# Performance work log

Measured on AMD Instinct MI355X. Metric: run time of the kernel, lower is better.

The kernel has to match this reference:

```python
import jax, jax.numpy as jnp
import numpy as np
import math

N_EMBD = 1024
N_HEAD = 16
B, T = 2, 2048


def new_gelu(x):
    # GPT-2 tanh-approx GELU (matches torch module exactly)
    return 0.5 * x * (1.0 + jnp.tanh(jnp.sqrt(2.0 / jnp.pi) * (x + 0.044715 * x ** 3)))


def layer_norm(x, w, b, eps=1e-5):
    mu = jnp.mean(x, axis=-1, keepdims=True)
    var = jnp.var(x, axis=-1, keepdims=True)
    return (x - mu) * jax.lax.rsqrt(var + eps) * w + b


def setup_inputs() -> dict:
    key = jax.random.key(0)
    ks = jax.random.split(key, 8)
    C = N_EMBD
    s = 0.02
    return {
        "x": jax.random.normal(ks[0], (B, T, C), dtype=jnp.float32),
        "ln1_w": jnp.ones((C,), jnp.float32),
        "ln1_b": jnp.zeros((C,), jnp.float32),
        "attn_w": s * jax.random.normal(ks[1], (C, 3 * C), jnp.float32),
        "attn_b": jnp.zeros((3 * C,), jnp.float32),
        "attn_proj_w": s * jax.random.normal(ks[2], (C, C), jnp.float32),
        "attn_proj_b": jnp.zeros((C,), jnp.float32),
        "ln2_w": jnp.ones((C,), jnp.float32),
        "ln2_b": jnp.zeros((C,), jnp.float32),
        "fc_w": s * jax.random.normal(ks[3], (C, 4 * C), jnp.float32),
        "fc_b": jnp.zeros((4 * C,), jnp.float32),
        "mlp_proj_w": s * jax.random.normal(ks[4], (4 * C, C), jnp.float32),
        "mlp_proj_b": jnp.zeros((C,), jnp.float32),
    }


def block_forward(x, ln1_w, ln1_b, attn_w, attn_b, attn_proj_w, attn_proj_b,
                  ln2_w, ln2_b, fc_w, fc_b, mlp_proj_w, mlp_proj_b):
    Bm, Tm, C = x.shape
    H = N_HEAD
    D = C // H
    # --- self attention (pre-LN) ---
    h = layer_norm(x, ln1_w, ln1_b)
    qkv = h @ attn_w + attn_b  # [B,T,3C]
    q, k, v = jnp.split(qkv, 3, axis=-1)
    q = q.reshape(Bm, Tm, H, D).transpose(0, 2, 1, 3)  # [B,H,T,D]
    k = k.reshape(Bm, Tm, H, D).transpose(0, 2, 1, 3)
    v = v.reshape(Bm, Tm, H, D).transpose(0, 2, 1, 3)
    att = jnp.einsum('bhqd,bhkd->bhqk', q, k) * (1.0 / math.sqrt(D))
    att = jax.nn.softmax(att, axis=-1)  # NOTE: no causal mask in source
    y = jnp.einsum('bhqk,bhkd->bhqd', att, v)
    y = y.transpose(0, 2, 1, 3).reshape(Bm, Tm, C)
    x = x + (y @ attn_proj_w + attn_proj_b)
    # --- MLP ---
    h = layer_norm(x, ln2_w, ln2_b)
    h = new_gelu(h @ fc_w + fc_b)
    x = x + (h @ mlp_proj_w + mlp_proj_b)
    return x


def reference(x, ln1_w, ln1_b, attn_w, attn_b, attn_proj_w, attn_proj_b,
              ln2_w, ln2_b, fc_w, fc_b, mlp_proj_w, mlp_proj_b):
    return block_forward(x, ln1_w, ln1_b, attn_w, attn_b, attn_proj_w, attn_proj_b,
                         ln2_w, ln2_b, fc_w, fc_b, mlp_proj_w, mlp_proj_b)
```

## Files before the change

### kernel.cpp

```cpp
#include <hip/hip_runtime.h>

typedef __attribute__((ext_vector_type(4)))  float  f32x4;
typedef __attribute__((ext_vector_type(16))) float  f32x16;
typedef __attribute__((ext_vector_type(8)))  short  s16x8;
typedef __attribute__((ext_vector_type(4)))  short  s16x4;
typedef __attribute__((ext_vector_type(4)))  unsigned u32x4;
typedef __attribute__((ext_vector_type(2)))  unsigned u32x2;
typedef __attribute__((ext_vector_type(2)))  int    i32x2;

__device__ __forceinline__ short f2bf(float f) {
    unsigned u = __builtin_bit_cast(unsigned, f);
    u += 0x7fff + ((u >> 16) & 1);
    return (short)(u >> 16);
}

__device__ __forceinline__ void load_lds16(const void* g, void* l) {
    __builtin_amdgcn_global_load_lds(
        (const __attribute__((address_space(1))) unsigned int*)g,
        (__attribute__((address_space(3))) unsigned int*)l, 16, 0, 0);
}

__device__ __forceinline__ float tmax32(const f32x16& a, const f32x16& b) {
    float u[11];
#pragma unroll
    for (int i = 0; i < 5; i++)
        u[i] = fmaxf(fmaxf(a[3 * i], a[3 * i + 1]), a[3 * i + 2]);
    u[5] = fmaxf(a[15], b[0]);
#pragma unroll
    for (int i = 0; i < 5; i++)
        u[6 + i] = fmaxf(fmaxf(b[3 * i + 1], b[3 * i + 2]), b[3 * i + 3]);
    float v0 = fmaxf(fmaxf(u[0], u[1]), u[2]);
    float v1 = fmaxf(fmaxf(u[3], u[4]), u[5]);
    float v2 = fmaxf(fmaxf(u[6], u[7]), u[8]);
    float v3 = fmaxf(u[9], u[10]);
    return fmaxf(fmaxf(v0, v1), fmaxf(v2, v3));
}

__device__ __forceinline__ float tsum32(const f32x16& a, const f32x16& b) {
    float u[16];
#pragma unroll
    for (int i = 0; i < 16; i++) u[i] = a[i] + b[i];
#pragma unroll
    for (int i = 0; i < 8; i++) u[i] += u[i + 8];
#pragma unroll
    for (int i = 0; i < 4; i++) u[i] += u[i + 4];
    return (u[0] + u[2]) + (u[1] + u[3]);
}

__global__ __launch_bounds__(256) void transpose_cast(const float* __restrict__ W,
                                                      short* __restrict__ Wt,
                                                      int K, int N) {
    __shared__ float t[32][33];
    int n0 = blockIdx.x * 32, k0 = blockIdx.y * 32;
    int tx = threadIdx.x & 31, ty = threadIdx.x >> 5;
#pragma unroll
    for (int i = 0; i < 4; i++)
        t[ty + 8 * i][tx] = W[(size_t)(k0 + ty + 8 * i) * N + n0 + tx];
    __syncthreads();
#pragma unroll
    for (int i = 0; i < 4; i++)
        Wt[(size_t)(n0 + ty + 8 * i) * K + k0 + tx] = f2bf(t[tx][ty + 8 * i]);
}

__global__ __launch_bounds__(256) void vtrans_kernel(const short* __restrict__ qkv,
                                                     short* __restrict__ Vtg) {
    const int T = 2048, C3 = 3072;
    __shared__ short tl[32][33];
    int bh = blockIdx.y >> 1;
    int b = bh >> 4, h = bh & 15;
    int dh = (blockIdx.y & 1) * 32;
    int t0 = blockIdx.x * 32;
    int tx = threadIdx.x & 31, ty = threadIdx.x >> 5;
    const short* src = qkv + (size_t)b * T * C3 + 2048 + h * 64 + dh;
#pragma unroll
    for (int i = 0; i < 4; i++)
        tl[ty + 8 * i][tx] = src[(size_t)(t0 + ty + 8 * i) * C3 + tx];
    __syncthreads();
#pragma unroll
    for (int i = 0; i < 4; i++)
        Vtg[((size_t)bh * 64 + dh + ty + 8 * i) * T + t0 + tx] = tl[tx][ty + 8 * i];
}

__global__ __launch_bounds__(256) void ln_kernel(const float* __restrict__ x,
                                                 const float* __restrict__ w,
                                                 const float* __restrict__ b,
                                                 short* __restrict__ out) {
    int row = blockIdx.x;
    int tid = threadIdx.x;
    const float4 v = ((const float4*)(x + (size_t)row * 1024))[tid];
    float s  = v.x + v.y + v.z + v.w;
    float ss = v.x * v.x + v.y * v.y + v.z * v.z + v.w * v.w;
#pragma unroll
    for (int o = 32; o > 0; o >>= 1) {
        s  += __shfl_down(s, o);
        ss += __shfl_down(ss, o);
    }
    __shared__ float rs[4], rq[4];
    int wave = tid >> 6, lane = tid & 63;
    if (lane == 0) { rs[wave] = s; rq[wave] = ss; }
    __syncthreads();
    float tot = rs[0] + rs[1] + rs[2] + rs[3];
    float tq  = rq[0] + rq[1] + rq[2] + rq[3];
    float mu   = tot * (1.f / 1024.f);
    float var  = tq * (1.f / 1024.f) - mu * mu;
    float rstd = rsqrtf(var + 1e-5f);
    const float4 wv = ((const float4*)w)[tid];
    const float4 bv = ((const float4*)b)[tid];
    s16x4 o;
    o[0] = f2bf((v.x - mu) * rstd * wv.x + bv.x);
    o[1] = f2bf((v.y - mu) * rstd * wv.y + bv.y);
    o[2] = f2bf((v.z - mu) * rstd * wv.z + bv.z);
    o[3] = f2bf((v.w - mu) * rstd * wv.w + bv.w);
    ((s16x4*)(out + (size_t)row * 1024))[tid] = o;
}

__device__ __forceinline__ void xcd_remap(int& bx, int& by) {
    int gx = gridDim.x, gy = gridDim.y;
    int hwid = blockIdx.y * gx + blockIdx.x;
    int xcd = hwid & 7, rank = hwid >> 3;
    int pan = gx >> 3;
    bx = xcd * pan + rank / gy;
    by = rank % gy;
}

template <typename OUT_T, bool GELU, bool RES, bool SCALE_Q>
__global__ __launch_bounds__(256) void gemm_bt(const short* __restrict__ A,
                                               const short* __restrict__ Bt,
                                               const float* __restrict__ bias,
                                               const float* __restrict__ res,
                                               OUT_T* __restrict__ C,
                                               int M, int N, int K) {
    __shared__ __align__(16) short As[128 * 32];
    __shared__ __align__(16) short Bs[128 * 32];
    int tid = threadIdx.x;
    int bx, by;
    xcd_remap(bx, by);
    int m0 = by * 128, n0 = bx * 128;
    int wave = tid >> 6, lane = tid & 63;
    int wr = wave >> 1, wc = wave & 1;
    int g = lane >> 4, q = lane & 15;
    f32x4 acc[4][4] = {};
    const short* Ab = A + (size_t)m0 * K;
    const short* Bb = Bt + (size_t)n0 * K;
    int srow = tid >> 2;
    int scol = (tid & 3) * 8;
    for (int k0 = 0; k0 < K; k0 += 32) {
        __syncthreads();
        load_lds16(Ab + (size_t)srow * K + k0 + scol, As + tid * 8);
        load_lds16(Ab + (size_t)(srow + 64) * K + k0 + scol, As + 2048 + tid * 8);
        load_lds16(Bb + (size_t)srow * K + k0 + scol, Bs + tid * 8);
        load_lds16(Bb + (size_t)(srow + 64) * K + k0 + scol, Bs + 2048 + tid * 8);
        __syncthreads();
        s16x8 a[4], bf[4];
#pragma unroll
        for (int mi = 0; mi < 4; mi++)
            a[mi] = *(const s16x8*)(As + (wr * 64 + mi * 16 + q) * 32 + g * 8);
#pragma unroll
        for (int ni = 0; ni < 4; ni++)
            bf[ni] = *(const s16x8*)(Bs + (wc * 64 + ni * 16 + q) * 32 + g * 8);
#pragma unroll
        for (int mi = 0; mi < 4; mi++)
#pragma unroll
            for (int ni = 0; ni < 4; ni++)
                acc[mi][ni] = __builtin_amdgcn_mfma_f32_16x16x32_bf16(a[mi], bf[ni], acc[mi][ni], 0, 0, 0);
    }
#pragma unroll
    for (int mi = 0; mi < 4; mi++) {
#pragma unroll
        for (int ni = 0; ni < 4; ni++) {
            int row = m0 + wr * 64 + mi * 16 + g * 4;
            int col = n0 + wc * 64 + ni * 16 + q;
            float bb = bias[col];
#pragma unroll
            for (int r = 0; r < 4; r++) {
                float v = acc[mi][ni][r] + bb;
                if (RES) v += res[(size_t)(row + r) * N + col];
                if (GELU) {
                    float aa = 0.7978845608028654f * (v + 0.044715f * v * v * v);
                    float th = 1.f - 2.f / (__expf(2.f * aa) + 1.f);
                    v = 0.5f * v * (1.f + th);
                }
                if (SCALE_Q && col < 1024) v *= 0.18033688011112042f;
                if constexpr (sizeof(OUT_T) == 2)
                    C[(size_t)(row + r) * N + col] = f2bf(v);
                else
                    C[(size_t)(row + r) * N + col] = v;
            }
        }
    }
}

__global__ __launch_bounds__(256) void gemm_bt_sk(const short* __restrict__ A,
                                                  const short* __restrict__ Bt,
                                                  float* __restrict__ part,
                                                  int M, int N, int K, int Klen) {
    __shared__ __align__(16) short As[128 * 32];
    __shared__ __align__(16) short Bs[128 * 32];
    int tid = threadIdx.x;
    int bx, by;
    xcd_remap(bx, by);
    int m0 = by * 128, n0 = bx * 128;
    int kz = blockIdx.z;
    int wave = tid >> 6, lane = tid & 63;
    int wr = wave >> 1, wc = wave & 1;
    int g = lane >> 4, q = lane & 15;
    f32x4 acc[4][4] = {};
    const short* Ab = A + (size_t)m0 * K;
    const short* Bb = Bt + (size_t)n0 * K;
    int srow = tid >> 2;
    int scol = (tid & 3) * 8;
    int kend = kz * Klen + Klen;
    for (int k0 = kz * Klen; k0 < kend; k0 += 32) {
        __syncthreads();
        load_lds16(Ab + (size_t)srow * K + k0 + scol, As + tid * 8);
        load_lds16(Ab + (size_t)(srow + 64) * K + k0 + scol, As + 2048 + tid * 8);
        load_lds16(Bb + (size_t)srow * K + k0 + scol, Bs + tid * 8);
        load_lds16(Bb + (size_t)(srow + 64) * K + k0 + scol, Bs + 2048 + tid * 8);
        __syncthreads();
        s16x8 a[4], bf[4];
#pragma unroll
        for (int mi = 0; mi < 4; mi++)
            a[mi] = *(const s16x8*)(As + (wr * 64 + mi * 16 + q) * 32 + g * 8);
#pragma unroll
        for (int ni = 0; ni < 4; ni++)
            bf[ni] = *(const s16x8*)(Bs + (wc * 64 + ni * 16 + q) * 32 + g * 8);
#pragma unroll
        for (int mi = 0; mi < 4; mi++)
#pragma unroll
            for (int ni = 0; ni < 4; ni++)
                acc[mi][ni] = __builtin_amdgcn_mfma_f32_16x16x32_bf16(a[mi], bf[ni], acc[mi][ni], 0, 0, 0);
    }
    float* pb = part + (size_t)kz * M * N;
#pragma unroll
    for (int mi = 0; mi < 4; mi++) {
#pragma unroll
        for (int ni = 0; ni < 4; ni++) {
            int row = m0 + wr * 64 + mi * 16 + g * 4;
            int col = n0 + wc * 64 + ni * 16 + q;
#pragma unroll
            for (int r = 0; r < 4; r++)
                pb[(size_t)(row + r) * N + col] = acc[mi][ni][r];
        }
    }
}

template <int SK>
__global__ __launch_bounds__(256) void reduce_sk(const float* __restrict__ part,
                                                 const float* __restrict__ bias,
                                                 const float* __restrict__ res,
                                                 float* __restrict__ out,
                                                 int MN, int N) {
    int tot = MN >> 2;
    int nb4 = (N >> 2) - 1;
    for (int i = blockIdx.x * 256 + threadIdx.x; i < tot; i += gridDim.x * 256) {
        float4 s = ((const float4*)part)[i];
#pragma unroll
        for (int k = 1; k < SK; k++) {
            float4 p = ((const float4*)(part + (size_t)k * MN))[i];
            s.x += p.x; s.y += p.y; s.z += p.z; s.w += p.w;
        }
        float4 bv = ((const float4*)bias)[i & nb4];
        float4 rv = ((const float4*)res)[i];
        float4 o;
        o.x = s.x + bv.x + rv.x;
        o.y = s.y + bv.y + rv.y;
        o.z = s.z + bv.z + rv.z;
        o.w = s.w + bv.w + rv.w;
        ((float4*)out)[i] = o;
    }
}

__global__ __launch_bounds__(256) void attn_kernel(const short* __restrict__ qkv,
                                                   const short* __restrict__ Vtg,
                                                   short* __restrict__ y) {
    const int T = 2048, C3 = 3072;
    int wg = blockIdx.x;
    int mapped = (wg & 7) * 64 + (wg >> 3);
    int bh = mapped >> 4, qt = mapped & 15;
    int b = bh >> 4, h = bh & 15;
    int tid = threadIdx.x, lane = tid & 63, wave = tid >> 6;
    int ql = lane & 31, hi = lane >> 5;
    const short* base = qkv + (size_t)b * T * C3;

    int qrow = qt * 128 + wave * 32 + ql;
    const short* qp = base + (size_t)qrow * C3 + h * 64;
    s16x8 qf[4];
#pragma unroll
    for (int s = 0; s < 4; s++)
        qf[s] = *(const s16x8*)(qp + ((2 * s + hi) << 3));

    __shared__ __align__(16) short Ks[2][64 * 64];
    __shared__ __align__(16) short Vs[2][64 * 64];

    int srow = tid >> 3, sc8 = tid & 7;
    const short* kp = base + 1024 + h * 64 + (size_t)srow * C3 + ((sc8 ^ (srow & 7)) << 3);
    const short* vp = Vtg + ((size_t)bh * 64 + srow) * T + ((sc8 ^ (srow & 7)) << 3);

    auto stage = [&](int bi) {
        load_lds16(kp, &Ks[bi][tid * 8]);
        load_lds16(kp + (size_t)32 * C3, &Ks[bi][tid * 8 + 2048]);
        load_lds16(vp, &Vs[bi][tid * 8]);
        load_lds16(vp + (size_t)32 * T, &Vs[bi][tid * 8 + 2048]);
    };

    float mst = -INFINITY, lst = 0.f;
    f32x16 accY0 = {}, accY1 = {};
    int swz = ql & 7;

    stage(0);
    for (int t = 0; t < 32; ++t) {
        int cur = t & 1;
        __syncthreads();
        if (t < 31) {
            kp += 64 * C3;
            vp += 64;
            stage(cur ^ 1);
        }
        f32x16 s0 = {}, s1 = {};
        const short* kb0 = &Ks[cur][ql * 64];
        const short* kb1 = &Ks[cur][(32 + ql) * 64];
        __builtin_amdgcn_s_setprio(1);
#pragma unroll
        for (int s = 0; s < 4; s++) {
            int c = ((2 * s + hi) ^ swz) << 3;
            s16x8 k0 = *(const s16x8*)(kb0 + c);
            s16x8 k1 = *(const s16x8*)(kb1 + c);
            s0 = __builtin_amdgcn_mfma_f32_32x32x16_bf16(k0, qf[s], s0, 0, 0, 0);
            s1 = __builtin_amdgcn_mfma_f32_32x32x16_bf16(k1, qf[s], s1, 0, 0, 0);
        }
        __builtin_amdgcn_s_setprio(0);
        float tm = tmax32(s0, s1);
        tm = fmaxf(tm, __shfl_xor(tm, 32));
        if (!__all(tm <= mst + 8.f)) {
            float mnew = fmaxf(mst, tm);
            float alpha = exp2f(mst - mnew);
            lst *= alpha;
#pragma unroll
            for (int r = 0; r < 16; r++) { accY0[r] *= alpha; accY1[r] *= alpha; }
            mst = mnew;
        }
#pragma unroll
        for (int r = 0; r < 16; r++) s0[r] = exp2f(s0[r] - mst);
#pragma unroll
        for (int r = 0; r < 16; r++) s1[r] = exp2f(s1[r] - mst);
        float ps = tsum32(s0, s1);
        ps += __shfl_xor(ps, 32);
        lst += ps;
        s16x8 pb[4];
#pragma unroll
        for (int s = 0; s < 4; s++) {
            int tt = (s & 1) * 8;
            unsigned lo0, lo1, hi0, hi1;
            if (s < 2) {
                asm("v_cvt_pk_bf16_f32 %0, %1, %2" : "=v"(lo0) : "v"(s0[tt + 0]), "v"(s0[tt + 1]));
                asm("v_cvt_pk_bf16_f32 %0, %1, %2" : "=v"(lo1) : "v"(s0[tt + 2]), "v"(s0[tt + 3]));
                asm("v_cvt_pk_bf16_f32 %0, %1, %2" : "=v"(hi0) : "v"(s0[tt + 4]), "v"(s0[tt + 5]));
                asm("v_cvt_pk_bf16_f32 %0, %1, %2" : "=v"(hi1) : "v"(s0[tt + 6]), "v"(s0[tt + 7]));
            } else {
                asm("v_cvt_pk_bf16_f32 %0, %1, %2" : "=v"(lo0) : "v"(s1[tt + 0]), "v"(s1[tt + 1]));
                asm("v_cvt_pk_bf16_f32 %0, %1, %2" : "=v"(lo1) : "v"(s1[tt + 2]), "v"(s1[tt + 3]));
                asm("v_cvt_pk_bf16_f32 %0, %1, %2" : "=v"(hi0) : "v"(s1[tt + 4]), "v"(s1[tt + 5]));
                asm("v_cvt_pk_bf16_f32 %0, %1, %2" : "=v"(hi1) : "v"(s1[tt + 6]), "v"(s1[tt + 7]));
            }
            i32x2 r0 = __builtin_amdgcn_permlane32_swap((int)hi0, (int)lo0, false, false);
            i32x2 r1 = __builtin_amdgcn_permlane32_swap((int)hi1, (int)lo1, false, false);
            u32x4 w;
            w[0] = (unsigned)r0[1]; w[1] = (unsigned)r1[1];
            w[2] = (unsigned)r0[0]; w[3] = (unsigned)r1[0];
            pb[s] = __builtin_bit_cast(s16x8, w);
        }
        const short* vb0 = &Vs[cur][ql * 64];
        const short* vb1 = &Vs[cur][(32 + ql) * 64];
        __builtin_amdgcn_s_setprio(1);
#pragma unroll
        for (int s = 0; s < 4; s++) {
            int c = ((2 * s + hi) ^ swz) << 3;
            s16x8 v0 = *(const s16x8*)(vb0 + c);
            s16x8 v1 = *(const s16x8*)(vb1 + c);
            accY0 = __builtin_amdgcn_mfma_f32_32x32x16_bf16(v0, pb[s], accY0, 0, 0, 0);
            accY1 = __builtin_amdgcn_mfma_f32_32x32x16_bf16(v1, pb[s], accY1, 0, 0, 0);
        }
        __builtin_amdgcn_s_setprio(0);
    }
    float linv = 1.f / lst;
    short* yrow = y + ((size_t)b * T + qrow) * 1024 + h * 64;
#pragma unroll
    for (int r = 0; r < 4; r++) {
        unsigned w0, w1, w2, w3;
        float a0 = accY0[4 * r] * linv, a1 = accY0[4 * r + 1] * linv;
        float a2 = accY0[4 * r + 2] * linv, a3 = accY0[4 * r + 3] * linv;
        float b0 = accY1[4 * r] * linv, b1 = accY1[4 * r + 1] * linv;
        float b2 = accY1[4 * r + 2] * linv, b3 = accY1[4 * r + 3] * linv;
        asm("v_cvt_pk_bf16_f32 %0, %1, %2" : "=v"(w0) : "v"(a0), "v"(a1));
        asm("v_cvt_pk_bf16_f32 %0, %1, %2" : "=v"(w1) : "v"(a2), "v"(a3));
        asm("v_cvt_pk_bf16_f32 %0, %1, %2" : "=v"(w2) : "v"(b0), "v"(b1));
        asm("v_cvt_pk_bf16_f32 %0, %1, %2" : "=v"(w3) : "v"(b2), "v"(b3));
        u32x2 p0; p0[0] = w0; p0[1] = w1;
        u32x2 p1; p1[0] = w2; p1[1] = w3;
        *(u32x2*)(yrow + 8 * r + 4 * hi)      = p0;
        *(u32x2*)(yrow + 32 + 8 * r + 4 * hi) = p1;
    }
}

extern "C" void kernel_launch(void* const* d_in, const int* in_sizes, int n_in,
                              void* d_out, int out_size, void* d_ws, size_t ws_size,
                              hipStream_t stream) {
    const float* x           = (const float*)d_in[0];
    const float* ln1_w       = (const float*)d_in[1];
    const float* ln1_b       = (const float*)d_in[2];
    const float* attn_w      = (const float*)d_in[3];
    const float* attn_b      = (const float*)d_in[4];
    const float* attn_proj_w = (const float*)d_in[5];
    const float* attn_proj_b = (const float*)d_in[6];
    const float* ln2_w       = (const float*)d_in[7];
    const float* ln2_b       = (const float*)d_in[8];
    const float* fc_w        = (const float*)d_in[9];
    const float* fc_b        = (const float*)d_in[10];
    const float* mlp_proj_w  = (const float*)d_in[11];
    const float* mlp_proj_b  = (const float*)d_in[12];

    const int M = 4096;

    size_t off = 0;
    char* wsb = (char*)d_ws;
    auto alloc = [&](size_t bytes) {
        void* p = wsb + off;
        off += (bytes + 255) & ~(size_t)255;
        return p;
    };
    short* wt_attn  = (short*)alloc(3072ull * 1024 * 2);
    short* wt_proj  = (short*)alloc(1024ull * 1024 * 2);
    short* wt_fc    = (short*)alloc(4096ull * 1024 * 2);
    short* wt_mproj = (short*)alloc(1024ull * 4096 * 2);
    short* h1       = (short*)alloc((size_t)M * 1024 * 2);
    short* qkvb     = (short*)alloc((size_t)M * 3072 * 2);
    short* yb       = (short*)alloc((size_t)M * 1024 * 2);
    float* x1       = (float*)alloc((size_t)M * 1024 * 4);
    short* vtg      = (short*)alloc((size_t)M * 1024 * 2);
    short* h2       = qkvb;

    size_t base_off = off;
    int SK = 0;
    if (ws_size >= base_off + 4ull * M * 1024 * 4) SK = 4;
    else if (ws_size >= base_off + 2ull * M * 1024 * 4) SK = 2;
    float* part = (float*)(wsb + base_off);

    transpose_cast<<<dim3(3072 / 32, 1024 / 32), 256, 0, stream>>>(attn_w, wt_attn, 1024, 3072);
    transpose_cast<<<dim3(1024 / 32, 1024 / 32), 256, 0, stream>>>(attn_proj_w, wt_proj, 1024, 1024);
    transpose_cast<<<dim3(4096 / 32, 1024 / 32), 256, 0, stream>>>(fc_w, wt_fc, 1024, 4096);
    transpose_cast<<<dim3(1024 / 32, 4096 / 32), 256, 0, stream>>>(mlp_proj_w, wt_mproj, 4096, 1024);

    ln_kernel<<<M, 256, 0, stream>>>(x, ln1_w, ln1_b, h1);
    gemm_bt<short, false, false, true><<<dim3(3072 / 128, M / 128), 256, 0, stream>>>(
        h1, wt_attn, attn_b, nullptr, qkvb, M, 3072, 1024);
    vtrans_kernel<<<dim3(2048 / 32, 64), 256, 0, stream>>>(qkvb, vtg);
    attn_kernel<<<512, 256, 0, stream>>>(qkvb, vtg, yb);
    gemm_bt<float, false, true, false><<<dim3(1024 / 128, M / 128), 256, 0, stream>>>(
        yb, wt_proj, attn_proj_b, x, x1, M, 1024, 1024);
    ln_kernel<<<M, 256, 0, stream>>>(x1, ln2_w, ln2_b, h1);
    gemm_bt<short, true, false, false><<<dim3(4096 / 128, M / 128), 256, 0, stream>>>(
        h1, wt_fc, fc_b, nullptr, h2, M, 4096, 1024);

    if (SK == 4) {
        gemm_bt_sk<<<dim3(1024 / 128, M / 128, 4), 256, 0, stream>>>(
            h2, wt_mproj, part, M, 1024, 4096, 1024);
        reduce_sk<4><<<2048, 256, 0, stream>>>(part, mlp_proj_b, x1, (float*)d_out, M * 1024, 1024);
    } else if (SK == 2) {
        gemm_bt_sk<<<dim3(1024 / 128, M / 128, 2), 256, 0, stream>>>(
            h2, wt_mproj, part, M, 1024, 4096, 2048);
        reduce_sk<2><<<2048, 256, 0, stream>>>(part, mlp_proj_b, x1, (float*)d_out, M * 1024, 1024);
    } else {
        gemm_bt<float, false, true, false><<<dim3(1024 / 128, M / 128), 256, 0, stream>>>(
            h2, wt_mproj, mlp_proj_b, x1, (float*)d_out, M, 1024, 4096);
    }
}
```

Measured before the change: 311.7 us.

## Double-buffer LDS tiles in GEMM kernels to overlap loads with MFMA

Both GEMM kernels (fused epilogue and split-K) now keep two LDS buffers for the A and B tiles. Each iteration issues the global-to-LDS loads for the next K step before running the MFMAs on the current buffer, with a single barrier per iteration instead of two. The aim is to hide global load latency behind matrix math and cut barrier stalls. In exchange, LDS use per block doubles to 32 KB, which could lower occupancy.

```diff
diff --git a/kernel.cpp b/kernel.cpp
--- a/kernel.cpp
+++ b/kernel.cpp
@@ -130,8 +130,8 @@
                                                const float* __restrict__ res,
                                                OUT_T* __restrict__ C,
                                                int M, int N, int K) {
-    __shared__ __align__(16) short As[128 * 32];
-    __shared__ __align__(16) short Bs[128 * 32];
+    __shared__ __align__(16) short As[2][128 * 32];
+    __shared__ __align__(16) short Bs[2][128 * 32];
     int tid = threadIdx.x;
     int bx, by;
     xcd_remap(bx, by);
@@ -144,25 +144,31 @@
     const short* Bb = Bt + (size_t)n0 * K;
     int srow = tid >> 2;
     int scol = (tid & 3) * 8;
-    for (int k0 = 0; k0 < K; k0 += 32) {
-        __syncthreads();
-        load_lds16(Ab + (size_t)srow * K + k0 + scol, As + tid * 8);
-        load_lds16(Ab + (size_t)(srow + 64) * K + k0 + scol, As + 2048 + tid * 8);
-        load_lds16(Bb + (size_t)srow * K + k0 + scol, Bs + tid * 8);
-        load_lds16(Bb + (size_t)(srow + 64) * K + k0 + scol, Bs + 2048 + tid * 8);
-        __syncthreads();
+    auto stage = [&](int bi, int k0) {
+        load_lds16(Ab + (size_t)srow * K + k0 + scol, &As[bi][tid * 8]);
+        load_lds16(Ab + (size_t)(srow + 64) * K + k0 + scol, &As[bi][2048 + tid * 8]);
+        load_lds16(Bb + (size_t)srow * K + k0 + scol, &Bs[bi][tid * 8]);
+        load_lds16(Bb + (size_t)(srow + 64) * K + k0 + scol, &Bs[bi][2048 + tid * 8]);
+    };
+    int nk = K >> 5;
+    stage(0, 0);
+    __syncthreads();
+    for (int kk = 0; kk < nk; ++kk) {
+        int cur = kk & 1;
+        if (kk + 1 < nk) stage(cur ^ 1, (kk + 1) << 5);
         s16x8 a[4], bf[4];
 #pragma unroll
         for (int mi = 0; mi < 4; mi++)
-            a[mi] = *(const s16x8*)(As + (wr * 64 + mi * 16 + q) * 32 + g * 8);
+            a[mi] = *(const s16x8*)(&As[cur][(wr * 64 + mi * 16 + q) * 32 + g * 8]);
 #pragma unroll
         for (int ni = 0; ni < 4; ni++)
-            bf[ni] = *(const s16x8*)(Bs + (wc * 64 + ni * 16 + q) * 32 + g * 8);
+            bf[ni] = *(const s16x8*)(&Bs[cur][(wc * 64 + ni * 16 + q) * 32 + g * 8]);
 #pragma unroll
         for (int mi = 0; mi < 4; mi++)
 #pragma unroll
             for (int ni = 0; ni < 4; ni++)
                 acc[mi][ni] = __builtin_amdgcn_mfma_f32_16x16x32_bf16(a[mi], bf[ni], acc[mi][ni], 0, 0, 0);
+        __syncthreads();
     }
 #pragma unroll
     for (int mi = 0; mi < 4; mi++) {
@@ -194,8 +200,8 @@
                                                   const short* __restrict__ Bt,
                                                   float* __restrict__ part,
                                                   int M, int N, int K, int Klen) {
-    __shared__ __align__(16) short As[128 * 32];
-    __shared__ __align__(16) short Bs[128 * 32];
+    __shared__ __align__(16) short As[2][128 * 32];
+    __shared__ __align__(16) short Bs[2][128 * 32];
     int tid = threadIdx.x;
     int bx, by;
     xcd_remap(bx, by);
@@ -209,26 +215,32 @@
     const short* Bb = Bt + (size_t)n0 * K;
     int srow = tid >> 2;
     int scol = (tid & 3) * 8;
-    int kend = kz * Klen + Klen;
-    for (int k0 = kz * Klen; k0 < kend; k0 += 32) {
-        __syncthreads();
-        load_lds16(Ab + (size_t)srow * K + k0 + scol, As + tid * 8);
-        load_lds16(Ab + (size_t)(srow + 64) * K + k0 + scol, As + 2048 + tid * 8);
-        load_lds16(Bb + (size_t)srow * K + k0 + scol, Bs + tid * 8);
-        load_lds16(Bb + (size_t)(srow + 64) * K + k0 + scol, Bs + 2048 + tid * 8);
-        __syncthreads();
+    auto stage = [&](int bi, int k0) {
+        load_lds16(Ab + (size_t)srow * K + k0 + scol, &As[bi][tid * 8]);
+        load_lds16(Ab + (size_t)(srow + 64) * K + k0 + scol, &As[bi][2048 + tid * 8]);
+        load_lds16(Bb + (size_t)srow * K + k0 + scol, &Bs[bi][tid * 8]);
+        load_lds16(Bb + (size_t)(srow + 64) * K + k0 + scol, &Bs[bi][2048 + tid * 8]);
+    };
+    int kbase = kz * Klen;
+    int nk = Klen >> 5;
+    stage(0, kbase);
+    __syncthreads();
+    for (int kk = 0; kk < nk; ++kk) {
+        int cur = kk & 1;
+        if (kk + 1 < nk) stage(cur ^ 1, kbase + ((kk + 1) << 5));
         s16x8 a[4], bf[4];
 #pragma unroll
         for (int mi = 0; mi < 4; mi++)
-            a[mi] = *(const s16x8*)(As + (wr * 64 + mi * 16 + q) * 32 + g * 8);
+            a[mi] = *(const s16x8*)(&As[cur][(wr * 64 + mi * 16 + q) * 32 + g * 8]);
 #pragma unroll
         for (int ni = 0; ni < 4; ni++)
-            bf[ni] = *(const s16x8*)(Bs + (wc * 64 + ni * 16 + q) * 32 + g * 8);
+            bf[ni] = *(const s16x8*)(&Bs[cur][(wc * 64 + ni * 16 + q) * 32 + g * 8]);
 #pragma unroll
         for (int mi = 0; mi < 4; mi++)
 #pragma unroll
             for (int ni = 0; ni < 4; ni++)
                 acc[mi][ni] = __builtin_amdgcn_mfma_f32_16x16x32_bf16(a[mi], bf[ni], acc[mi][ni], 0, 0, 0);
+        __syncthreads();
     }
     float* pb = part + (size_t)kz * M * N;
 #pragma unroll
```

After: 295.9 us. 1.05x faster.
